# Kernel optimization log

Measured on AMD Instinct MI355X. Metric: run time of the kernel, lower is better.

The kernel has to match this reference:

```python
import jax, jax.numpy as jnp
import numpy as np

NUM_GROUPS = 32
NUM_FEATURES = 256
EPS = 1e-5


def setup_inputs() -> dict:
    key = jax.random.key(0)
    x = jax.random.normal(key, (32, NUM_FEATURES, 64, 64), dtype=jnp.float32)
    gamma = jnp.ones((NUM_FEATURES,), jnp.float32)
    beta = jnp.zeros((NUM_FEATURES,), jnp.float32)
    return {"x": x, "gamma": gamma, "beta": beta}


def reference(x, gamma, beta):
    B, C, H, W = x.shape
    k = NUM_FEATURES // NUM_GROUPS  # channels per dynamic group
    # --- cosine similarity across channels (training path) ---
    x_flat = x.reshape(B, C, H * W)
    nrm = jnp.linalg.norm(x_flat, axis=2, keepdims=True)
    x_n = x_flat / jnp.maximum(nrm, 1e-12)  # F.normalize semantics
    cos = jnp.einsum('bcn,bdn->cd', x_n, x_n) / B  # mean over batch, [C,C]
    # torch.topk(|cos|, k, dim=0, largest=False): per-column k smallest.
    # Row c of |cos|.T is column c, so lax.top_k of -|cos|.T gives idx[c,i]=top_inds[i,c].
    _, idx = jax.lax.top_k(-jnp.abs(cos).T, k)  # [C, k]
    # --- group statistics without materializing [B,C,k,H,W] ---
    s = x.sum(axis=(2, 3))          # [B,C] per-channel spatial sum
    sq = (x * x).sum(axis=(2, 3))   # [B,C]
    # group = channel c itself + channels idx[c,1:]  (idx[:,0] replaced by x in original)
    gs = s + s[:, idx[:, 1:]].sum(axis=-1)    # [B,C]
    gsq = sq + sq[:, idx[:, 1:]].sum(axis=-1)  # [B,C]
    N = k * H * W
    mean = gs / N
    var = gsq / N - mean * mean  # unbiased=False
    inv = jax.lax.rsqrt(var + EPS)
    x_hat = (x - mean[:, :, None, None]) * inv[:, :, None, None]
    return gamma[None, :, None, None] * x_hat + beta[None, :, None, None]
```

## Files before the change

### kernel.cpp

```cpp
#include <hip/hip_runtime.h>
#include <math.h>

#define BATCH 32
#define CH 256
#define HW 4096
#define KSEL 8
#define EPSV 1e-5f

typedef __attribute__((ext_vector_type(8))) short short8;
typedef __attribute__((ext_vector_type(4))) float f32x4;

__device__ __forceinline__ unsigned short f2bf(float f) {
    unsigned u = __float_as_uint(f);
    unsigned r = u + 0x7fffu + ((u >> 16) & 1u);
    return (unsigned short)(r >> 16);
}
__device__ __forceinline__ float bf2f(unsigned short h) {
    return __uint_as_float(((unsigned)h) << 16);
}

__global__ __launch_bounds__(512, 2) void gram256(const float* __restrict__ x,
                                                  float* __restrict__ cosP,
                                                  float* __restrict__ sP,
                                                  float* __restrict__ sqP) {
    int z = blockIdx.x;
    int b = z >> 3, q = z & 7;
    const float* xb = x + (size_t)b * CH * HW;

    __shared__ unsigned short Hh[CH * 72];
    __shared__ unsigned short Hl[CH * 72];

    int t = threadIdx.x, lane = t & 63, w = t >> 6;
    int wr = (w >> 2) * 128, wc = (w & 3) * 64;
    int fr = lane & 15, fg = lane >> 4;

    int rt = t >> 1, hf = t & 1;

    float sl = 0.f, sql = 0.f;
    f32x4 acc[8][4] = {};

    for (int kb = 0; kb < 8; ++kb) {
        const float4* src = (const float4*)(xb + (size_t)rt * HW + q * 512 + kb * 64 + hf * 32);
        float4 f[8];
#pragma unroll
        for (int i = 0; i < 8; ++i) f[i] = src[i];
        __syncthreads();
#pragma unroll
        for (int p = 0; p < 4; ++p) {
            float a[8];
            a[0] = f[2 * p].x;     a[1] = f[2 * p].y;
            a[2] = f[2 * p].z;     a[3] = f[2 * p].w;
            a[4] = f[2 * p + 1].x; a[5] = f[2 * p + 1].y;
            a[6] = f[2 * p + 1].z; a[7] = f[2 * p + 1].w;
            short8 hv, lv;
#pragma unroll
            for (int j = 0; j < 8; ++j) {
                sl += a[j];
                sql += a[j] * a[j];
                unsigned short h = f2bf(a[j]);
                hv[j] = (short)h;
                lv[j] = (short)f2bf(2.0f * (a[j] - bf2f(h)));
            }
            int addr = rt * 72 + (hf * 4 + p) * 8;
            *(short8*)&Hh[addr] = hv;
            *(short8*)&Hl[addr] = lv;
        }
        __syncthreads();
#pragma unroll
        for (int ks = 0; ks < 2; ++ks) {
            int gk = ks * 4 + fg;
            short8 af[8], bh[4], bl[4];
#pragma unroll
            for (int mi = 0; mi < 8; ++mi)
                af[mi] = *(const short8*)&Hh[(wr + mi * 16 + fr) * 72 + gk * 8];
#pragma unroll
            for (int nj = 0; nj < 4; ++nj) {
                int rb = (wc + nj * 16 + fr) * 72 + gk * 8;
                bh[nj] = *(const short8*)&Hh[rb];
                bl[nj] = *(const short8*)&Hl[rb];
            }
#pragma unroll
            for (int mi = 0; mi < 8; ++mi)
#pragma unroll
                for (int nj = 0; nj < 4; ++nj) {
                    acc[mi][nj] = __builtin_amdgcn_mfma_f32_16x16x32_bf16(af[mi], bh[nj], acc[mi][nj], 0, 0, 0);
                    acc[mi][nj] = __builtin_amdgcn_mfma_f32_16x16x32_bf16(af[mi], bl[nj], acc[mi][nj], 0, 0, 0);
                }
        }
    }

    sl += __shfl_down(sl, 1);
    sql += __shfl_down(sql, 1);
    if (hf == 0) {
        sP[(size_t)z * CH + rt] = sl;
        sqP[(size_t)z * CH + rt] = sql;
    }

    float* Cp = cosP + (size_t)z * CH * CH;
#pragma unroll
    for (int mi = 0; mi < 8; ++mi)
#pragma unroll
        for (int nj = 0; nj < 4; ++nj) {
#pragma unroll
            for (int reg = 0; reg < 4; ++reg) {
                int r = wr + mi * 16 + fg * 4 + reg;
                int c = wc + nj * 16 + fr;
                Cp[(size_t)r * CH + c] = acc[mi][nj][reg];
            }
        }
}

__global__ __launch_bounds__(256) void finalize_kernel(const float* __restrict__ sP,
                                                       const float* __restrict__ sqP,
                                                       float* __restrict__ s,
                                                       float* __restrict__ sq,
                                                       float* __restrict__ invn) {
    int b = blockIdx.x, c = threadIdx.x;
    float S = 0.f, Q = 0.f;
#pragma unroll
    for (int q = 0; q < 8; ++q) {
        S += sP[(size_t)(b * 8 + q) * CH + c];
        Q += sqP[(size_t)(b * 8 + q) * CH + c];
    }
    s[b * CH + c] = S;
    sq[b * CH + c] = Q;
    invn[b * CH + c] = 1.0f / fmaxf(sqrtf(Q), 1e-12f);
}

__global__ __launch_bounds__(1024) void reduceP(const float* __restrict__ cosP,
                                                const float* __restrict__ invn,
                                                float* __restrict__ R) {
    int r = blockIdx.x;
    int t = threadIdx.x;
    int d = t & 255, pg = t >> 8;
    const float* base = cosP + (size_t)r * CH + d;
    float acc = 0.f;
    for (int b = pg * 8; b < pg * 8 + 8; ++b) {
        float part = 0.f;
#pragma unroll
        for (int q = 0; q < 8; ++q)
            part += base[(size_t)(b * 8 + q) * (CH * CH)];
        acc += part * invn[b * CH + d] * invn[b * CH + r];
    }
    __shared__ float red[1024];
    red[t] = acc;
    __syncthreads();
    if (t < 256)
        R[(size_t)r * CH + t] = red[t] + red[t + 256] + red[t + 512] + red[t + 768];
}

__global__ __launch_bounds__(256) void symtopk(const float* __restrict__ R,
                                               int* __restrict__ idx) {
    int c = blockIdx.x;
    int d = threadIdx.x;
    float v = fabsf((R[(size_t)c * CH + d] + R[(size_t)d * CH + c]) * (0.5f / BATCH));

    __shared__ unsigned long long keys[CH];
    __shared__ unsigned long long wmin[4];
    __shared__ unsigned long long bmin;

    keys[d] = ((unsigned long long)__float_as_uint(v) << 32) | (unsigned)d;
    __syncthreads();

    for (int i = 0; i < KSEL; ++i) {
        unsigned long long k = keys[d];
        for (int off = 32; off; off >>= 1) {
            unsigned long long o = __shfl_down(k, off);
            k = (o < k) ? o : k;
        }
        if ((d & 63) == 0) wmin[d >> 6] = k;
        __syncthreads();
        if (d == 0) {
            unsigned long long m = wmin[0];
            if (wmin[1] < m) m = wmin[1];
            if (wmin[2] < m) m = wmin[2];
            if (wmin[3] < m) m = wmin[3];
            bmin = m;
            idx[c * KSEL + i] = (int)(m & 0xffffffffu);
        }
        __syncthreads();
        int sel = (int)(bmin & 0xffffffffu);
        if (d == sel) keys[d] = 0xffffffffffffffffULL;
        __syncthreads();
    }
}

__global__ __launch_bounds__(256) void groupstat_kernel(const float* __restrict__ s,
                                                        const float* __restrict__ sq,
                                                        const int* __restrict__ idx,
                                                        float* __restrict__ mean,
                                                        float* __restrict__ inv) {
    int b = blockIdx.x, c = threadIdx.x;
    float gs = s[b * CH + c], gq = sq[b * CH + c];
#pragma unroll
    for (int i = 1; i < KSEL; ++i) {
        int d = idx[c * KSEL + i];
        gs += s[b * CH + d];
        gq += sq[b * CH + d];
    }
    const float Ninv = 1.0f / (float)(KSEL * HW);
    float m = gs * Ninv;
    float var = gq * Ninv - m * m;
    mean[b * CH + c] = m;
    inv[b * CH + c]  = rsqrtf(var + EPSV);
}

__global__ __launch_bounds__(256) void norm_kernel(const float* __restrict__ x,
                                                   const float* __restrict__ mean,
                                                   const float* __restrict__ inv,
                                                   const float* __restrict__ gamma,
                                                   const float* __restrict__ beta,
                                                   float* __restrict__ out) {
    int i = blockIdx.x * 256 + threadIdx.x;
    int bc = i >> 10;
    int c  = bc & (CH - 1);
    float m = mean[bc], v = inv[bc];
    float g  = gamma[c] * v;
    float bt = beta[c] - m * g;
    float4 xv = ((const float4*)x)[i];
    float4 o;
    o.x = xv.x * g + bt;
    o.y = xv.y * g + bt;
    o.z = xv.z * g + bt;
    o.w = xv.w * g + bt;
    ((float4*)out)[i] = o;
}

extern "C" void kernel_launch(void* const* d_in, const int* in_sizes, int n_in,
                              void* d_out, int out_size, void* d_ws, size_t ws_size,
                              hipStream_t stream) {
    const float* x     = (const float*)d_in[0];
    const float* gamma = (const float*)d_in[1];
    const float* beta  = (const float*)d_in[2];
    float* out = (float*)d_out;

    float* cosP = (float*)d_out;

    float* ws   = (float*)d_ws;
    float* sP   = ws;
    float* sqP  = sP + 256 * CH;
    float* s    = sqP + 256 * CH;
    float* sq   = s + BATCH * CH;
    float* invn = sq + BATCH * CH;
    float* mean = invn + BATCH * CH;
    float* inv  = mean + BATCH * CH;
    float* R    = inv + BATCH * CH;
    int*   idx  = (int*)(R + CH * CH);

    gram256<<<256, 512, 0, stream>>>(x, cosP, sP, sqP);
    finalize_kernel<<<BATCH, 256, 0, stream>>>(sP, sqP, s, sq, invn);
    reduceP<<<CH, 1024, 0, stream>>>(cosP, invn, R);
    symtopk<<<CH, 256, 0, stream>>>(R, idx);
    groupstat_kernel<<<BATCH, 256, 0, stream>>>(s, sq, idx, mean, inv);
    norm_kernel<<<(BATCH * CH * HW / 4) / 256, 256, 0, stream>>>(x, mean, inv, gamma, beta, out);
}
```

Baseline: 118.7 us.

## Double-buffer global loads, coalesce reads, swizzle LDS, truncate bf16 split in gram kernel

Measured after the change: 214.2 us. 80.4% more time.

```diff
diff --git a/kernel.cpp b/kernel.cpp
--- a/kernel.cpp
+++ b/kernel.cpp
@@ -10,16 +10,7 @@
 typedef __attribute__((ext_vector_type(8))) short short8;
 typedef __attribute__((ext_vector_type(4))) float f32x4;
 
-__device__ __forceinline__ unsigned short f2bf(float f) {
-    unsigned u = __float_as_uint(f);
-    unsigned r = u + 0x7fffu + ((u >> 16) & 1u);
-    return (unsigned short)(r >> 16);
-}
-__device__ __forceinline__ float bf2f(unsigned short h) {
-    return __uint_as_float(((unsigned)h) << 16);
-}
-
-__global__ __launch_bounds__(512, 2) void gram256(const float* __restrict__ x,
+__global__ __launch_bounds__(512, 1) void gram256(const float* __restrict__ x,
                                                   float* __restrict__ cosP,
                                                   float* __restrict__ sP,
                                                   float* __restrict__ sqP) {
@@ -27,73 +18,98 @@
     int b = z >> 3, q = z & 7;
     const float* xb = x + (size_t)b * CH * HW;
 
-    __shared__ unsigned short Hh[CH * 72];
-    __shared__ unsigned short Hl[CH * 72];
+    __shared__ unsigned short Hh[CH * 64];
+    __shared__ unsigned short Hl[CH * 64];
 
     int t = threadIdx.x, lane = t & 63, w = t >> 6;
     int wr = (w >> 2) * 128, wc = (w & 3) * 64;
     int fr = lane & 15, fg = lane >> 4;
 
-    int rt = t >> 1, hf = t & 1;
-
-    float sl = 0.f, sql = 0.f;
+    int rowbase = t >> 4;
+    int col16 = t & 15;
+    int gr = col16 >> 1;
+    int halfo = (col16 & 1) * 4;
+    const float4* srcb4 = (const float4*)xb + (size_t)rowbase * (HW / 4) + q * 128 + col16;
+
+    float sl[8] = {}, sql[8] = {};
     f32x4 acc[8][4] = {};
-
-    for (int kb = 0; kb < 8; ++kb) {
-        const float4* src = (const float4*)(xb + (size_t)rt * HW + q * 512 + kb * 64 + hf * 32);
-        float4 f[8];
-#pragma unroll
-        for (int i = 0; i < 8; ++i) f[i] = src[i];
-        __syncthreads();
-#pragma unroll
-        for (int p = 0; p < 4; ++p) {
-            float a[8];
-            a[0] = f[2 * p].x;     a[1] = f[2 * p].y;
-            a[2] = f[2 * p].z;     a[3] = f[2 * p].w;
-            a[4] = f[2 * p + 1].x; a[5] = f[2 * p + 1].y;
-            a[6] = f[2 * p + 1].z; a[7] = f[2 * p + 1].w;
-            short8 hv, lv;
-#pragma unroll
-            for (int j = 0; j < 8; ++j) {
-                sl += a[j];
-                sql += a[j] * a[j];
-                unsigned short h = f2bf(a[j]);
-                hv[j] = (short)h;
-                lv[j] = (short)f2bf(2.0f * (a[j] - bf2f(h)));
-            }
-            int addr = rt * 72 + (hf * 4 + p) * 8;
-            *(short8*)&Hh[addr] = hv;
-            *(short8*)&Hl[addr] = lv;
-        }
-        __syncthreads();
-#pragma unroll
-        for (int ks = 0; ks < 2; ++ks) {
-            int gk = ks * 4 + fg;
-            short8 af[8], bh[4], bl[4];
-#pragma unroll
-            for (int mi = 0; mi < 8; ++mi)
-                af[mi] = *(const short8*)&Hh[(wr + mi * 16 + fr) * 72 + gk * 8];
-#pragma unroll
-            for (int nj = 0; nj < 4; ++nj) {
-                int rb = (wc + nj * 16 + fr) * 72 + gk * 8;
-                bh[nj] = *(const short8*)&Hh[rb];
-                bl[nj] = *(const short8*)&Hl[rb];
-            }
-#pragma unroll
-            for (int mi = 0; mi < 8; ++mi)
-#pragma unroll
-                for (int nj = 0; nj < 4; ++nj) {
-                    acc[mi][nj] = __builtin_amdgcn_mfma_f32_16x16x32_bf16(af[mi], bh[nj], acc[mi][nj], 0, 0, 0);
-                    acc[mi][nj] = __builtin_amdgcn_mfma_f32_16x16x32_bf16(af[mi], bl[nj], acc[mi][nj], 0, 0, 0);
-                }
-        }
-    }
-
-    sl += __shfl_down(sl, 1);
-    sql += __shfl_down(sql, 1);
-    if (hf == 0) {
-        sP[(size_t)z * CH + rt] = sl;
-        sqP[(size_t)z * CH + rt] = sql;
+    float4 fA[8], fB[8];
+
+#define LOAD8(FB, KB) { const float4* sp = srcb4 + (size_t)(KB) * 16;              \
+    _Pragma("unroll") for (int i = 0; i < 8; ++i) FB[i] = sp[(size_t)i * 32768]; }
+
+#define CONVERT8(FB) { _Pragma("unroll") for (int i = 0; i < 8; ++i) {             \
+    float4 v = FB[i];                                                              \
+    sl[i] += v.x + v.y + v.z + v.w;                                                \
+    sql[i] += v.x * v.x + v.y * v.y + v.z * v.z + v.w * v.w;                       \
+    unsigned u0 = __float_as_uint(v.x), u1 = __float_as_uint(v.y);                 \
+    unsigned u2 = __float_as_uint(v.z), u3 = __float_as_uint(v.w);                 \
+    unsigned hp0 = (u0 >> 16) | (u1 & 0xffff0000u);                                \
+    unsigned hp1 = (u2 >> 16) | (u3 & 0xffff0000u);                                \
+    float lo0 = v.x - __uint_as_float(u0 & 0xffff0000u);                           \
+    float lo1 = v.y - __uint_as_float(u1 & 0xffff0000u);                           \
+    float lo2 = v.z - __uint_as_float(u2 & 0xffff0000u);                           \
+    float lo3 = v.w - __uint_as_float(u3 & 0xffff0000u);                           \
+    lo0 += lo0; lo1 += lo1; lo2 += lo2; lo3 += lo3;                                \
+    unsigned lp0 = (__float_as_uint(lo0) >> 16) | (__float_as_uint(lo1) & 0xffff0000u); \
+    unsigned lp1 = (__float_as_uint(lo2) >> 16) | (__float_as_uint(lo3) & 0xffff0000u); \
+    int r = rowbase + 32 * i;                                                      \
+    int adr = r * 64 + ((gr ^ (r & 7)) * 8) + halfo;                               \
+    *(uint2*)&Hh[adr] = make_uint2(hp0, hp1);                                      \
+    *(uint2*)&Hl[adr] = make_uint2(lp0, lp1);                                      \
+} }
+
+#define MFMA_PHASE { _Pragma("unroll") for (int ks = 0; ks < 2; ++ks) {            \
+    int gk = ks * 4 + fg;                                                          \
+    short8 af[8], bh[4], bl[4];                                                    \
+    _Pragma("unroll") for (int mi = 0; mi < 8; ++mi) {                             \
+        int r = wr + mi * 16 + fr;                                                 \
+        af[mi] = *(const short8*)&Hh[r * 64 + ((gk ^ (r & 7)) * 8)];               \
+    }                                                                              \
+    _Pragma("unroll") for (int nj = 0; nj < 4; ++nj) {                             \
+        int r = wc + nj * 16 + fr;                                                 \
+        int rb = r * 64 + ((gk ^ (r & 7)) * 8);                                    \
+        bh[nj] = *(const short8*)&Hh[rb];                                          \
+        bl[nj] = *(const short8*)&Hl[rb];                                          \
+    }                                                                              \
+    _Pragma("unroll") for (int mi = 0; mi < 8; ++mi)                               \
+        _Pragma("unroll") for (int nj = 0; nj < 4; ++nj) {                         \
+            acc[mi][nj] = __builtin_amdgcn_mfma_f32_16x16x32_bf16(af[mi], bh[nj], acc[mi][nj], 0, 0, 0); \
+            acc[mi][nj] = __builtin_amdgcn_mfma_f32_16x16x32_bf16(af[mi], bl[nj], acc[mi][nj], 0, 0, 0); \
+        }                                                                          \
+} }
+
+    LOAD8(fA, 0)
+    LOAD8(fB, 1)
+#pragma unroll
+    for (int kb2 = 0; kb2 < 4; ++kb2) {
+        __syncthreads();
+        CONVERT8(fA)
+        if (kb2 < 3) LOAD8(fA, 2 * kb2 + 2)
+        __syncthreads();
+        MFMA_PHASE
+        __syncthreads();
+        CONVERT8(fB)
+        if (kb2 < 3) LOAD8(fB, 2 * kb2 + 3)
+        __syncthreads();
+        MFMA_PHASE
+    }
+
+#pragma unroll
+    for (int i = 0; i < 8; ++i) {
+#pragma unroll
+        for (int off = 1; off < 16; off <<= 1) {
+            sl[i] += __shfl_xor(sl[i], off);
+            sql[i] += __shfl_xor(sql[i], off);
+        }
+    }
+    if ((t & 15) == 0) {
+#pragma unroll
+        for (int i = 0; i < 8; ++i) {
+            int r = rowbase + 32 * i;
+            sP[(size_t)z * CH + r] = sl[i];
+            sqP[(size_t)z * CH + r] = sql[i];
+        }
     }
 
     float* Cp = cosP + (size_t)z * CH * CH;
@@ -108,6 +124,9 @@
                 Cp[(size_t)r * CH + c] = acc[mi][nj][reg];
             }
         }
+#undef LOAD8
+#undef CONVERT8
+#undef MFMA_PHASE
 }
 
 __global__ __launch_bounds__(256) void finalize_kernel(const float* __restrict__ sP,
```

## Double-buffer gram loads via direct global-to-LDS with swizzled bf16 split

Applied to the files above, without the earlier changes.

Measured after the change: 108.5 us. 1.09x faster.

```diff
diff --git a/kernel.cpp b/kernel.cpp
--- a/kernel.cpp
+++ b/kernel.cpp
@@ -10,16 +10,12 @@
 typedef __attribute__((ext_vector_type(8))) short short8;
 typedef __attribute__((ext_vector_type(4))) float f32x4;
 
-__device__ __forceinline__ unsigned short f2bf(float f) {
-    unsigned u = __float_as_uint(f);
-    unsigned r = u + 0x7fffu + ((u >> 16) & 1u);
-    return (unsigned short)(r >> 16);
-}
-__device__ __forceinline__ float bf2f(unsigned short h) {
-    return __uint_as_float(((unsigned)h) << 16);
-}
-
-__global__ __launch_bounds__(512, 2) void gram256(const float* __restrict__ x,
+__device__ __forceinline__ void gload16(const void* g, void* l) {
+    __builtin_amdgcn_global_load_lds((const __attribute__((address_space(1))) void*)g,
+                                     (__attribute__((address_space(3))) void*)l, 16, 0, 0);
+}
+
+__global__ __launch_bounds__(512, 1) void gram256(const float* __restrict__ x,
                                                   float* __restrict__ cosP,
                                                   float* __restrict__ sP,
                                                   float* __restrict__ sqP) {
@@ -27,73 +23,102 @@
     int b = z >> 3, q = z & 7;
     const float* xb = x + (size_t)b * CH * HW;
 
-    __shared__ unsigned short Hh[CH * 72];
-    __shared__ unsigned short Hl[CH * 72];
+    __shared__ float4 ldsF[2][2048];
+    __shared__ unsigned short Hh[CH * 32];
+    __shared__ unsigned short Hl[CH * 32];
 
     int t = threadIdx.x, lane = t & 63, w = t >> 6;
     int wr = (w >> 2) * 128, wc = (w & 3) * 64;
     int fr = lane & 15, fg = lane >> 4;
-
-    int rt = t >> 1, hf = t & 1;
-
-    float sl = 0.f, sql = 0.f;
+    int rl = lane >> 3;
+    int gs = lane & 7;
+    int kbase = q * 512;
+
+    float sl[4] = {}, sql[4] = {};
     f32x4 acc[8][4] = {};
 
-    for (int kb = 0; kb < 8; ++kb) {
-        const float4* src = (const float4*)(xb + (size_t)rt * HW + q * 512 + kb * 64 + hf * 32);
-        float4 f[8];
-#pragma unroll
-        for (int i = 0; i < 8; ++i) f[i] = src[i];
-        __syncthreads();
-#pragma unroll
-        for (int p = 0; p < 4; ++p) {
-            float a[8];
-            a[0] = f[2 * p].x;     a[1] = f[2 * p].y;
-            a[2] = f[2 * p].z;     a[3] = f[2 * p].w;
-            a[4] = f[2 * p + 1].x; a[5] = f[2 * p + 1].y;
-            a[6] = f[2 * p + 1].z; a[7] = f[2 * p + 1].w;
-            short8 hv, lv;
-#pragma unroll
-            for (int j = 0; j < 8; ++j) {
-                sl += a[j];
-                sql += a[j] * a[j];
-                unsigned short h = f2bf(a[j]);
-                hv[j] = (short)h;
-                lv[j] = (short)f2bf(2.0f * (a[j] - bf2f(h)));
-            }
-            int addr = rt * 72 + (hf * 4 + p) * 8;
-            *(short8*)&Hh[addr] = hv;
-            *(short8*)&Hl[addr] = lv;
-        }
-        __syncthreads();
-#pragma unroll
-        for (int ks = 0; ks < 2; ++ks) {
-            int gk = ks * 4 + fg;
-            short8 af[8], bh[4], bl[4];
-#pragma unroll
-            for (int mi = 0; mi < 8; ++mi)
-                af[mi] = *(const short8*)&Hh[(wr + mi * 16 + fr) * 72 + gk * 8];
-#pragma unroll
-            for (int nj = 0; nj < 4; ++nj) {
-                int rb = (wc + nj * 16 + fr) * 72 + gk * 8;
-                bh[nj] = *(const short8*)&Hh[rb];
-                bl[nj] = *(const short8*)&Hl[rb];
-            }
-#pragma unroll
-            for (int mi = 0; mi < 8; ++mi)
-#pragma unroll
-                for (int nj = 0; nj < 4; ++nj) {
-                    acc[mi][nj] = __builtin_amdgcn_mfma_f32_16x16x32_bf16(af[mi], bh[nj], acc[mi][nj], 0, 0, 0);
-                    acc[mi][nj] = __builtin_amdgcn_mfma_f32_16x16x32_bf16(af[mi], bl[nj], acc[mi][nj], 0, 0, 0);
-                }
-        }
-    }
-
-    sl += __shfl_down(sl, 1);
-    sql += __shfl_down(sql, 1);
-    if (hf == 0) {
-        sP[(size_t)z * CH + rt] = sl;
-        sqP[(size_t)z * CH + rt] = sql;
+#define ISSUE(KB, BUF) {                                                          \
+    int k0 = kbase + (KB) * 32;                                                   \
+    _Pragma("unroll") for (int j = 0; j < 4; ++j) {                               \
+        int row = w * 32 + j * 8 + rl;                                            \
+        const float* src = xb + (size_t)row * HW + k0 + ((gs ^ rl) * 4);          \
+        gload16(src, &ldsF[BUF][(w * 4 + j) * 64]);                               \
+    } }
+
+#define CONVERT(BUF) {                                                            \
+    _Pragma("unroll") for (int j = 0; j < 4; ++j) {                               \
+        float4 v = ldsF[BUF][(w * 4 + j) * 64 + lane];                            \
+        int row = w * 32 + j * 8 + rl;                                            \
+        int G = gs ^ rl;                                                          \
+        sl[j] += v.x + v.y + v.z + v.w;                                           \
+        sql[j] += v.x * v.x + v.y * v.y + v.z * v.z + v.w * v.w;                  \
+        unsigned u0 = __float_as_uint(v.x), u1 = __float_as_uint(v.y);            \
+        unsigned u2 = __float_as_uint(v.z), u3 = __float_as_uint(v.w);            \
+        unsigned hp0 = (u0 >> 16) | (u1 & 0xffff0000u);                           \
+        unsigned hp1 = (u2 >> 16) | (u3 & 0xffff0000u);                           \
+        float lo0 = v.x - __uint_as_float(u0 & 0xffff0000u);                      \
+        float lo1 = v.y - __uint_as_float(u1 & 0xffff0000u);                      \
+        float lo2 = v.z - __uint_as_float(u2 & 0xffff0000u);                      \
+        float lo3 = v.w - __uint_as_float(u3 & 0xffff0000u);                      \
+        lo0 += lo0; lo1 += lo1; lo2 += lo2; lo3 += lo3;                           \
+        unsigned lp0 = (__float_as_uint(lo0) >> 16) | (__float_as_uint(lo1) & 0xffff0000u); \
+        unsigned lp1 = (__float_as_uint(lo2) >> 16) | (__float_as_uint(lo3) & 0xffff0000u); \
+        int adr = row * 32 + (((G >> 1) ^ (row & 3)) * 8) + (G & 1) * 4;          \
+        *(uint2*)&Hh[adr] = make_uint2(hp0, hp1);                                 \
+        *(uint2*)&Hl[adr] = make_uint2(lp0, lp1);                                 \
+    } }
+
+#define MFMA_PHASE {                                                              \
+    short8 af[8], bh[4], bl[4];                                                   \
+    _Pragma("unroll") for (int mi = 0; mi < 8; ++mi) {                            \
+        int r = wr + mi * 16 + fr;                                                \
+        af[mi] = *(const short8*)&Hh[r * 32 + ((fg ^ (r & 3)) * 8)];              \
+    }                                                                             \
+    _Pragma("unroll") for (int nj = 0; nj < 4; ++nj) {                            \
+        int r = wc + nj * 16 + fr;                                                \
+        int adr = r * 32 + ((fg ^ (r & 3)) * 8);                                  \
+        bh[nj] = *(const short8*)&Hh[adr];                                        \
+        bl[nj] = *(const short8*)&Hl[adr];                                        \
+    }                                                                             \
+    _Pragma("unroll") for (int mi = 0; mi < 8; ++mi)                              \
+        _Pragma("unroll") for (int nj = 0; nj < 4; ++nj) {                        \
+            acc[mi][nj] = __builtin_amdgcn_mfma_f32_16x16x32_bf16(af[mi], bh[nj], acc[mi][nj], 0, 0, 0); \
+            acc[mi][nj] = __builtin_amdgcn_mfma_f32_16x16x32_bf16(af[mi], bl[nj], acc[mi][nj], 0, 0, 0); \
+        } }
+
+    ISSUE(0, 0)
+#pragma unroll 2
+    for (int kb = 0; kb < 16; ++kb) {
+        if (kb < 15) {
+            ISSUE(kb + 1, (kb + 1) & 1)
+            asm volatile("s_waitcnt vmcnt(4)" ::: "memory");
+        } else {
+            asm volatile("s_waitcnt vmcnt(0)" ::: "memory");
+        }
+        __builtin_amdgcn_sched_barrier(0);
+        __builtin_amdgcn_s_barrier();
+        CONVERT(kb & 1)
+        asm volatile("s_waitcnt lgkmcnt(0)" ::: "memory");
+        __builtin_amdgcn_sched_barrier(0);
+        __builtin_amdgcn_s_barrier();
+        MFMA_PHASE
+    }
+
+#pragma unroll
+    for (int j = 0; j < 4; ++j) {
+#pragma unroll
+        for (int off = 1; off < 8; off <<= 1) {
+            sl[j] += __shfl_xor(sl[j], off);
+            sql[j] += __shfl_xor(sql[j], off);
+        }
+    }
+    if (gs == 0) {
+#pragma unroll
+        for (int j = 0; j < 4; ++j) {
+            int row = w * 32 + j * 8 + rl;
+            sP[(size_t)z * CH + row] = sl[j];
+            sqP[(size_t)z * CH + row] = sql[j];
+        }
     }
 
     float* Cp = cosP + (size_t)z * CH * CH;
@@ -108,6 +133,9 @@
                 Cp[(size_t)r * CH + c] = acc[mi][nj][reg];
             }
         }
+#undef ISSUE
+#undef CONVERT
+#undef MFMA_PHASE
 }
 
 __global__ __launch_bounds__(256) void finalize_kernel(const float* __restrict__ sP,
```
